# Kernel tuning notes

Measured on AMD Instinct MI355X. Metric: run time of the kernel, lower is better.

Reference implementation:

```python
import jax, jax.numpy as jnp
import numpy as np

B, D, H = 8192, 256, 1024


def setup_inputs() -> dict:
    key = jax.random.key(0)
    ks = jax.random.split(key, 24)
    glorot = lambda k, o, i: jax.random.uniform(k, (o, i), jnp.float32, -1.0, 1.0) * jnp.sqrt(6.0 / (o + i))
    inp = {
        'x': jax.random.normal(ks[0], (B, D), jnp.float32),
        'm': (jax.random.uniform(ks[1], (B, D)) < 0.8).astype(jnp.float32),  # binary observation mask
        'delta': jax.random.uniform(ks[2], (B, D), jnp.float32),             # nonnegative time gaps
        'h': jax.random.normal(ks[3], (B, H), jnp.float32),
        'x_last_obs': jax.random.normal(ks[4], (B, D), jnp.float32),
        'x_mean': jax.random.normal(ks[5], (D,), jnp.float32),
        'W_gamma_x': jax.random.uniform(ks[6], (D,), jnp.float32, 0.001, 0.01),
        'b_gamma_x': jnp.zeros((D,), jnp.float32),
        'W_gamma_h': glorot(ks[7], H, D), 'b_gamma_h': jnp.zeros((H,), jnp.float32),
        'W_xz': glorot(ks[8], H, D), 'W_hz': glorot(ks[9], H, H),
        'W_mz': glorot(ks[10], H, D), 'b_mz': jnp.zeros((H,), jnp.float32),
        'W_xr': glorot(ks[11], H, D), 'W_hr': glorot(ks[12], H, H),
        'W_mr': glorot(ks[13], H, D), 'b_mr': jnp.zeros((H,), jnp.float32),
        'W_xh': glorot(ks[14], H, D), 'W_hh': glorot(ks[15], H, H),
        'W_mh': glorot(ks[16], H, D), 'b_mh': jnp.zeros((H,), jnp.float32),
    }
    return inp


def reference(x, m, delta, h, x_last_obs, x_mean,
              W_gamma_x, b_gamma_x, W_gamma_h, b_gamma_h,
              W_xz, W_hz, W_mz, b_mz,
              W_xr, W_hr, W_mr, b_mr,
              W_xh, W_hh, W_mh, b_mh):
    # input decay (per-feature) and hidden decay (linear of delta)
    gamma_x = jnp.exp(-jax.nn.relu(delta * W_gamma_x + b_gamma_x))        # [B, D]
    gamma_h = jnp.exp(-jax.nn.relu(delta @ W_gamma_h.T + b_gamma_h))     # [B, H]
    # imputation
    x_last_obs_new = jnp.where(m > 0, x, x_last_obs)
    x_imputed = gamma_x * x_last_obs_new + (1.0 - gamma_x) * x_mean
    x_hat = m * x + (1.0 - m) * x_imputed
    h_decayed = gamma_h * h
    # GRU gates (eval mode: no recurrent dropout)
    z = jax.nn.sigmoid(x_hat @ W_xz.T + h_decayed @ W_hz.T + m @ W_mz.T + b_mz)
    r = jax.nn.sigmoid(x_hat @ W_xr.T + h_decayed @ W_hr.T + m @ W_mr.T + b_mr)
    h_tilde = jnp.tanh(x_hat @ W_xh.T + (r * h_decayed) @ W_hh.T + m @ W_mh.T + b_mh)
    h_new = (1.0 - z) * h_decayed + z * h_tilde
    return h_new, x_last_obs_new
```

## Files before the change

kernel.cpp:

```cpp
#include <hip/hip_runtime.h>
#include <cstdint>
#include <cstddef>

typedef unsigned short u16;
typedef __attribute__((ext_vector_type(8))) short s16x8;
typedef __attribute__((ext_vector_type(8))) u16 u16x8;
typedef __attribute__((ext_vector_type(4))) float f32x4;

#define DEV static __device__ __forceinline__
#define GPTR(p) (const __attribute__((address_space(1))) void*)(p)
#define LPTR(p) (__attribute__((address_space(3))) void*)(p)

DEV float b2f(u16 u) { union { unsigned i; float f; } c; c.i = ((unsigned)u) << 16; return c.f; }
DEV u16 f2b(float f) {
  union { float f; unsigned i; } c; c.f = f;
  unsigned r = (c.i + 0x7fffu + ((c.i >> 16) & 1u)) >> 16;
  return (u16)r;
}
DEV float sigm(float x) { return 1.0f / (1.0f + __expf(-x)); }

__global__ __launch_bounds__(256) void pack_w(
    const float* __restrict__ Wxz, const float* __restrict__ Whz, const float* __restrict__ Wmz,
    const float* __restrict__ Wxr, const float* __restrict__ Whr, const float* __restrict__ Wmr,
    const float* __restrict__ Wxh, const float* __restrict__ Whh, const float* __restrict__ Wmh,
    const float* __restrict__ Wgh,
    u16* __restrict__ WZR, u16* __restrict__ WH, u16* __restrict__ WGH)
{
  int t = blockIdx.x * 256 + threadIdx.x;
  const float* src;
  u16* dst;
  if (t < 589824) {
    int row = t / 192;
    int col = (t % 192) * 8;
    int rr = row & 1023;
    const float *wx, *wh, *wm;
    if (row < 1024)      { wx = Wxz; wh = Whz; wm = Wmz; }
    else if (row < 2048) { wx = Wxr; wh = Whr; wm = Wmr; }
    else                 { wx = Wxh; wh = Whh; wm = Wmh; }
    if (col < 256)       src = wx + rr * 256 + col;
    else if (col < 1280) src = wh + (size_t)rr * 1024 + (col - 256);
    else                 src = wm + rr * 256 + (col - 1280);
    dst = (row < 2048) ? (WZR + (size_t)row * 1536 + col)
                       : (WH + (size_t)(row - 2048) * 1536 + col);
  } else {
    int t2 = t - 589824;
    src = Wgh + t2 * 8;
    dst = WGH + t2 * 8;
  }
  f32x4 a = *(const f32x4*)src;
  f32x4 b = *(const f32x4*)(src + 4);
  u16x8 v;
#pragma unroll
  for (int j = 0; j < 4; ++j) { v[j] = f2b(a[j]); v[j + 4] = f2b(b[j]); }
  *(u16x8*)dst = v;
}

__global__ __launch_bounds__(256) void elem_k(
    const float* __restrict__ x, const float* __restrict__ m, const float* __restrict__ delta,
    const float* __restrict__ xlo, const float* __restrict__ x_mean,
    const float* __restrict__ Wgx, const float* __restrict__ bgx,
    u16* __restrict__ X1, u16* __restrict__ Dbf,
    float* __restrict__ out_xlo)
{
  int t = blockIdx.x * 256 + threadIdx.x;
  int row = t >> 5;
  int col = (t & 31) * 8;
  size_t base = (size_t)row * 256 + col;
  u16x8 vxhat, vm16, vd16;
  f32x4 vlnew[2];
#pragma unroll
  for (int half = 0; half < 2; ++half) {
    f32x4 vx = *(const f32x4*)(x + base + half * 4);
    f32x4 vm = *(const f32x4*)(m + base + half * 4);
    f32x4 vd = *(const f32x4*)(delta + base + half * 4);
    f32x4 vl = *(const f32x4*)(xlo + base + half * 4);
    f32x4 vmean = *(const f32x4*)(x_mean + col + half * 4);
    f32x4 vwg = *(const f32x4*)(Wgx + col + half * 4);
    f32x4 vbg = *(const f32x4*)(bgx + col + half * 4);
#pragma unroll
    for (int j = 0; j < 4; ++j) {
      float mf = vm[j];
      float lnew = (mf > 0.5f) ? vx[j] : vl[j];
      vlnew[half][j] = lnew;
      float gx = __expf(-fmaxf(vd[j] * vwg[j] + vbg[j], 0.0f));
      float ximp = gx * lnew + (1.0f - gx) * vmean[j];
      float xhat = mf * vx[j] + (1.0f - mf) * ximp;
      vxhat[half * 4 + j] = f2b(xhat);
      vm16[half * 4 + j] = f2b(mf);
      vd16[half * 4 + j] = f2b(vd[j]);
    }
  }
  size_t r1536 = (size_t)row * 1536;
  *(u16x8*)(X1 + r1536 + col) = vxhat;
  *(u16x8*)(X1 + r1536 + 1280 + col) = vm16;
  *(u16x8*)(Dbf + base) = vd16;
  *(f32x4*)(out_xlo + base) = vlnew[0];
  *(f32x4*)(out_xlo + base + 4) = vlnew[1];
}

template<int EPI, int MF>
__global__ __launch_bounds__(512, 2) void gemm_bt(
    const u16* __restrict__ A, const u16* __restrict__ A2, int K,
    const u16* __restrict__ W,
    const float* __restrict__ bias0, const float* __restrict__ bias1,
    const float* __restrict__ auxf,
    const u16* __restrict__ auxb,
    const u16* __restrict__ aux2b,
    u16* __restrict__ out0b,
    u16* __restrict__ out1b,
    float* __restrict__ outf)
{
  constexpr int BM = MF * 32;
  constexpr int GX = (MF == 8) ? 8 : 4;
  constexpr int LA = BM / 64;
  __shared__ alignas(16) u16 As[2][BM * 64];
  __shared__ alignas(16) u16 Bs[2][256 * 64];

  const int tid = threadIdx.x;
  const int lane = tid & 63;
  const int wave = tid >> 6;
  const int wr = wave >> 2;
  const int wc = wave & 3;

  const int d = blockIdx.y * GX + blockIdx.x;
  const int L = ((d & 7) << 5) | (d >> 3);
  const int brow = (L >> ((GX == 8) ? 3 : 2)) * BM;
  const int bcol = (L & (GX - 1)) * 256;
  const int NT = K / 64;

  const int slr = lane >> 3;
  const int scol = ((lane & 7) ^ slr) * 8;
  const int lr = lane & 15, g4 = lane >> 4, l8 = lane & 7;

  f32x4 acc[MF][4];
#pragma unroll
  for (int i = 0; i < MF; ++i)
#pragma unroll
    for (int j = 0; j < 4; ++j) { f32x4 z0 = {0.f, 0.f, 0.f, 0.f}; acc[i][j] = z0; }

  auto stageA = [&](int kt, int bu) {
    const int k0 = kt * 64;
    const u16* Ab; size_t Astr; int co = k0;
    if constexpr (EPI == 2) {
      if (kt >= 4 && kt < 20) { Ab = A2; Astr = 1024; co = k0 - 256; }
      else                    { Ab = A;  Astr = 1536; }
    } else { Ab = A; Astr = (size_t)K; }
#pragma unroll
    for (int j = 0; j < LA; ++j) {
      int rh = (j * 4 + wc) * 8;
      int grow = brow + wr * (BM / 2) + rh + slr;
      __builtin_amdgcn_global_load_lds(
          GPTR(Ab + (size_t)grow * Astr + co + scol),
          LPTR(&As[bu][(wr * (BM / 2) + rh) * 64]), 16, 0, 0);
    }
  };
  auto stageB = [&](int kt, int bu) {
    const int k0 = kt * 64;
    const int gw = wr * 2 + (wc & 1), hb = wc >> 1;
#pragma unroll
    for (int j = 0; j < 4; ++j) {
      int rh = (j * 4 + gw) * 8;
      int grow = bcol + hb * 128 + rh + slr;
      __builtin_amdgcn_global_load_lds(
          GPTR(W + (size_t)grow * (size_t)K + k0 + scol),
          LPTR(&Bs[bu][(hb * 128 + rh) * 64]), 16, 0, 0);
    }
  };

  stageA(0, 0); stageB(0, 0);
  asm volatile("s_waitcnt vmcnt(0)" ::: "memory");
  __builtin_amdgcn_s_barrier();

  for (int kt = 0; kt < NT; ++kt) {
    const int bu = kt & 1;
    const u16* as_ = &As[bu][0];
    const u16* bs_ = &Bs[bu][0];
    s16x8 bfr[4];
#pragma unroll
    for (int ks = 0; ks < 2; ++ks) {
#pragma unroll
      for (int ih = 0; ih < MF / 4; ++ih) {
        const int ph = ks * (MF / 4) + ih;
        const int kc = ((ks * 4 + g4) ^ l8) * 8;
        s16x8 af[4];
        if (ih == 0)
#pragma unroll
          for (int j = 0; j < 4; ++j)
            bfr[j] = *(const s16x8*)&bs_[(wc * 64 + j * 16 + lr) * 64 + kc];
#pragma unroll
        for (int ii = 0; ii < 4; ++ii)
          af[ii] = *(const s16x8*)&as_[(wr * (BM / 2) + (ih * 4 + ii) * 16 + lr) * 64 + kc];
        if (kt + 1 < NT) {
          if (ph == 0) { stageA(kt + 1, bu ^ 1); if (MF == 4) stageB(kt + 1, bu ^ 1); }
          else if (ph == 1 && MF == 8) stageB(kt + 1, bu ^ 1);
        }
        __builtin_amdgcn_sched_barrier(0);
        if (ph == 2 * (MF / 4) - 1 && kt + 1 < NT)
          asm volatile("s_waitcnt vmcnt(0)" ::: "memory");
        __builtin_amdgcn_s_barrier();
        asm volatile("s_waitcnt lgkmcnt(0)" ::: "memory");
        __builtin_amdgcn_sched_barrier(0);
        __builtin_amdgcn_s_setprio(1);
#pragma unroll
        for (int ii = 0; ii < 4; ++ii)
#pragma unroll
          for (int j = 0; j < 4; ++j)
            acc[ih * 4 + ii][j] = __builtin_amdgcn_mfma_f32_16x16x32_bf16(
                af[ii], bfr[j], acc[ih * 4 + ii][j], 0, 0, 0);
        __builtin_amdgcn_s_setprio(0);
        __builtin_amdgcn_sched_barrier(0);
        __builtin_amdgcn_s_barrier();
      }
    }
  }

  const int row0 = brow + wr * (MF * 16) + g4 * 4;
  const int col0 = bcol + wc * 64 + lr;
#pragma unroll
  for (int i = 0; i < MF; ++i) {
#pragma unroll
    for (int j = 0; j < 4; ++j) {
      int c_ = col0 + j * 16;
#pragma unroll
      for (int q = 0; q < 4; ++q) {
        int r_ = row0 + i * 16 + q;
        float v = acc[i][j][q];
        if constexpr (EPI == 0) {
          float p = v + bias0[c_];
          float gh = __expf(-fmaxf(p, 0.0f));
          float hd = gh * auxf[(size_t)r_ * 1024 + c_];
          out0b[(size_t)r_ * 1536 + 256 + c_] = f2b(hd);
        } else if constexpr (EPI == 1) {
          if (c_ < 1024) {
            out0b[(size_t)r_ * 1024 + c_] = f2b(sigm(v + bias0[c_]));
          } else {
            int jc = c_ - 1024;
            float rg = sigm(v + bias1[jc]);
            float hd = b2f(auxb[(size_t)r_ * 1536 + 256 + jc]);
            out1b[(size_t)r_ * 1024 + jc] = f2b(rg * hd);
          }
        } else {
          float ht = tanhf(v + bias0[c_]);
          float zz = b2f(aux2b[(size_t)r_ * 1024 + c_]);
          float hd = b2f(auxb[(size_t)r_ * 1536 + 256 + c_]);
          outf[(size_t)r_ * 1024 + c_] = (1.0f - zz) * hd + zz * ht;
        }
      }
    }
  }
}

extern "C" void kernel_launch(void* const* d_in, const int* in_sizes, int n_in,
                              void* d_out, int out_size, void* d_ws, size_t ws_size,
                              hipStream_t stream)
{
  const float* x     = (const float*)d_in[0];
  const float* m     = (const float*)d_in[1];
  const float* delta = (const float*)d_in[2];
  const float* h     = (const float*)d_in[3];
  const float* xlo   = (const float*)d_in[4];
  const float* xmean = (const float*)d_in[5];
  const float* Wgx   = (const float*)d_in[6];
  const float* bgx   = (const float*)d_in[7];
  const float* Wgh   = (const float*)d_in[8];
  const float* bgh   = (const float*)d_in[9];
  const float* Wxz   = (const float*)d_in[10];
  const float* Whz   = (const float*)d_in[11];
  const float* Wmz   = (const float*)d_in[12];
  const float* bmz   = (const float*)d_in[13];
  const float* Wxr   = (const float*)d_in[14];
  const float* Whr   = (const float*)d_in[15];
  const float* Wmr   = (const float*)d_in[16];
  const float* bmr   = (const float*)d_in[17];
  const float* Wxh   = (const float*)d_in[18];
  const float* Whh   = (const float*)d_in[19];
  const float* Wmh   = (const float*)d_in[20];
  const float* bmh   = (const float*)d_in[21];

  u16* X1  = (u16*)d_ws;
  u16* Z   = X1 + (size_t)8192 * 1536;
  u16* RH  = Z  + (size_t)8192 * 1024;
  u16* WZR = RH + (size_t)8192 * 1024;
  u16* WH  = WZR + (size_t)2048 * 1536;
  u16* Dbf = WH + (size_t)1024 * 1536;
  u16* WGH = Dbf + (size_t)8192 * 256;

  float* out_h   = (float*)d_out;
  float* out_xlo = out_h + (size_t)8192 * 1024;

  pack_w<<<2432, 256, 0, stream>>>(Wxz, Whz, Wmz, Wxr, Whr, Wmr, Wxh, Whh, Wmh, Wgh, WZR, WH, WGH);
  elem_k<<<1024, 256, 0, stream>>>(x, m, delta, xlo, xmean, Wgx, bgx, X1, Dbf, out_xlo);
  gemm_bt<0, 4><<<dim3(4, 64), 512, 0, stream>>>(
      Dbf, nullptr, 256, WGH, bgh, nullptr, h, nullptr, nullptr, X1, nullptr, nullptr);
  gemm_bt<1, 8><<<dim3(8, 32), 512, 0, stream>>>(
      X1, nullptr, 1536, WZR, bmz, bmr, nullptr, X1, nullptr, Z, RH, nullptr);
  gemm_bt<2, 4><<<dim3(4, 64), 512, 0, stream>>>(
      X1, RH, 1536, WH, bmh, nullptr, nullptr, X1, Z, nullptr, nullptr, out_h);
}
```

Measured before the change: 168.4 us.

## Split LDS tiles into K-halves and prefetch two stages ahead with partial waits

```diff
diff --git a/kernel.cpp b/kernel.cpp
--- a/kernel.cpp
+++ b/kernel.cpp
@@ -112,9 +112,10 @@
 {
   constexpr int BM = MF * 32;
   constexpr int GX = (MF == 8) ? 8 : 4;
-  constexpr int LA = BM / 64;
-  __shared__ alignas(16) u16 As[2][BM * 64];
-  __shared__ alignas(16) u16 Bs[2][256 * 64];
+  constexpr int AL = MF / 4;
+  constexpr int NPH = MF / 2;
+  __shared__ alignas(16) u16 As[2][2][BM * 32];
+  __shared__ alignas(16) u16 Bs[2][2][256 * 32];
 
   const int tid = threadIdx.x;
   const int lane = tid & 63;
@@ -124,13 +125,14 @@
 
   const int d = blockIdx.y * GX + blockIdx.x;
   const int L = ((d & 7) << 5) | (d >> 3);
-  const int brow = (L >> ((GX == 8) ? 3 : 2)) * BM;
-  const int bcol = (L & (GX - 1)) * 256;
+  const int brow = (L / GX) * BM;
+  const int bcol = (L % GX) * 256;
   const int NT = K / 64;
 
-  const int slr = lane >> 3;
-  const int scol = ((lane & 7) ^ slr) * 8;
-  const int lr = lane & 15, g4 = lane >> 4, l8 = lane & 7;
+  const int lr = lane & 15, g4 = lane >> 4;
+  const int rchunk = ((g4 ^ ((lr >> 1) & 3)) * 8);
+  const int sr16 = lane >> 2;
+  const int scs = (lane & 3) ^ ((sr16 >> 1) & 3);
 
   f32x4 acc[MF][4];
 #pragma unroll
@@ -138,79 +140,81 @@
 #pragma unroll
     for (int j = 0; j < 4; ++j) { f32x4 z0 = {0.f, 0.f, 0.f, 0.f}; acc[i][j] = z0; }
 
-  auto stageA = [&](int kt, int bu) {
-    const int k0 = kt * 64;
-    const u16* Ab; size_t Astr; int co = k0;
+  auto stA = [&](int st, int bu, int kh) {
+    int stc = st < NT ? st : NT - 1;
+    const u16* Ab; size_t Astr; int co;
     if constexpr (EPI == 2) {
-      if (kt >= 4 && kt < 20) { Ab = A2; Astr = 1024; co = k0 - 256; }
-      else                    { Ab = A;  Astr = 1536; }
-    } else { Ab = A; Astr = (size_t)K; }
-#pragma unroll
-    for (int j = 0; j < LA; ++j) {
-      int rh = (j * 4 + wc) * 8;
-      int grow = brow + wr * (BM / 2) + rh + slr;
+      if (stc >= 4 && stc < 20) { Ab = A2; Astr = 1024; co = stc * 64 + kh * 32 - 256; }
+      else                      { Ab = A;  Astr = 1536; co = stc * 64 + kh * 32; }
+    } else { Ab = A; Astr = (size_t)K; co = stc * 64 + kh * 32; }
+#pragma unroll
+    for (int q = 0; q < AL; ++q) {
+      int rb = (q * 8 + wave) * 16;
       __builtin_amdgcn_global_load_lds(
-          GPTR(Ab + (size_t)grow * Astr + co + scol),
-          LPTR(&As[bu][(wr * (BM / 2) + rh) * 64]), 16, 0, 0);
+          GPTR(Ab + (size_t)(brow + rb + sr16) * Astr + co + scs * 8),
+          LPTR(&As[bu][kh][rb * 32]), 16, 0, 0);
     }
   };
-  auto stageB = [&](int kt, int bu) {
-    const int k0 = kt * 64;
-    const int gw = wr * 2 + (wc & 1), hb = wc >> 1;
-#pragma unroll
-    for (int j = 0; j < 4; ++j) {
-      int rh = (j * 4 + gw) * 8;
-      int grow = bcol + hb * 128 + rh + slr;
+  auto stB = [&](int st, int bu, int kh) {
+    int stc = st < NT ? st : NT - 1;
+    int co = stc * 64 + kh * 32;
+#pragma unroll
+    for (int q = 0; q < 2; ++q) {
+      int rb = (q * 8 + wave) * 16;
       __builtin_amdgcn_global_load_lds(
-          GPTR(W + (size_t)grow * (size_t)K + k0 + scol),
-          LPTR(&Bs[bu][(hb * 128 + rh) * 64]), 16, 0, 0);
+          GPTR(W + (size_t)(bcol + rb + sr16) * (size_t)K + co + scs * 8),
+          LPTR(&Bs[bu][kh][rb * 32]), 16, 0, 0);
     }
   };
 
-  stageA(0, 0); stageB(0, 0);
-  asm volatile("s_waitcnt vmcnt(0)" ::: "memory");
+  stA(0, 0, 0); stB(0, 0, 0);
+  stA(0, 0, 1); stB(0, 0, 1);
+  stA(1, 1, 0); stB(1, 1, 0);
+  if constexpr (MF == 8) asm volatile("s_waitcnt vmcnt(8)" ::: "memory");
+  else                   asm volatile("s_waitcnt vmcnt(6)" ::: "memory");
   __builtin_amdgcn_s_barrier();
 
+  s16x8 bfr[4];
   for (int kt = 0; kt < NT; ++kt) {
     const int bu = kt & 1;
-    const u16* as_ = &As[bu][0];
-    const u16* bs_ = &Bs[bu][0];
-    s16x8 bfr[4];
-#pragma unroll
-    for (int ks = 0; ks < 2; ++ks) {
-#pragma unroll
-      for (int ih = 0; ih < MF / 4; ++ih) {
-        const int ph = ks * (MF / 4) + ih;
-        const int kc = ((ks * 4 + g4) ^ l8) * 8;
-        s16x8 af[4];
-        if (ih == 0)
-#pragma unroll
-          for (int j = 0; j < 4; ++j)
-            bfr[j] = *(const s16x8*)&bs_[(wc * 64 + j * 16 + lr) * 64 + kc];
-#pragma unroll
-        for (int ii = 0; ii < 4; ++ii)
-          af[ii] = *(const s16x8*)&as_[(wr * (BM / 2) + (ih * 4 + ii) * 16 + lr) * 64 + kc];
-        if (kt + 1 < NT) {
-          if (ph == 0) { stageA(kt + 1, bu ^ 1); if (MF == 4) stageB(kt + 1, bu ^ 1); }
-          else if (ph == 1 && MF == 8) stageB(kt + 1, bu ^ 1);
-        }
-        __builtin_amdgcn_sched_barrier(0);
-        if (ph == 2 * (MF / 4) - 1 && kt + 1 < NT)
-          asm volatile("s_waitcnt vmcnt(0)" ::: "memory");
-        __builtin_amdgcn_s_barrier();
-        asm volatile("s_waitcnt lgkmcnt(0)" ::: "memory");
-        __builtin_amdgcn_sched_barrier(0);
-        __builtin_amdgcn_s_setprio(1);
-#pragma unroll
-        for (int ii = 0; ii < 4; ++ii)
-#pragma unroll
-          for (int j = 0; j < 4; ++j)
-            acc[ih * 4 + ii][j] = __builtin_amdgcn_mfma_f32_16x16x32_bf16(
-                af[ii], bfr[j], acc[ih * 4 + ii][j], 0, 0, 0);
-        __builtin_amdgcn_s_setprio(0);
-        __builtin_amdgcn_sched_barrier(0);
-        __builtin_amdgcn_s_barrier();
+#pragma unroll
+    for (int ph = 0; ph < NPH; ++ph) {
+      const int ks = (MF == 8) ? (ph >> 1) : ph;
+      const int mq = (MF == 8) ? (ph & 1) : 0;
+      s16x8 af[4];
+      if (mq == 0)
+#pragma unroll
+        for (int j = 0; j < 4; ++j)
+          bfr[j] = *(const s16x8*)&Bs[bu][ks][(wc * 64 + j * 16 + lr) * 32 + rchunk];
+#pragma unroll
+      for (int ii = 0; ii < 4; ++ii)
+        af[ii] = *(const s16x8*)&As[bu][ks][(wr * (BM / 2) + mq * 64 + ii * 16 + lr) * 32 + rchunk];
+      if constexpr (MF == 8) {
+        if (ph == 0)      stA(kt + 1, bu ^ 1, 1);
+        else if (ph == 1) stB(kt + 1, bu ^ 1, 1);
+        else if (ph == 2) stA(kt + 2, bu, 0);
+        else              stB(kt + 2, bu, 0);
+      } else {
+        if (ph == 0) { stA(kt + 1, bu ^ 1, 1); stB(kt + 1, bu ^ 1, 1); }
+        else         { stA(kt + 2, bu, 0);     stB(kt + 2, bu, 0); }
       }
+      if constexpr (MF == 8) {
+        if (ph & 1) asm volatile("s_waitcnt vmcnt(8)" ::: "memory");
+      } else {
+        asm volatile("s_waitcnt vmcnt(6)" ::: "memory");
+      }
+      __builtin_amdgcn_s_barrier();
+      asm volatile("s_waitcnt lgkmcnt(0)" ::: "memory");
+      __builtin_amdgcn_sched_barrier(0);
+      __builtin_amdgcn_s_setprio(1);
+#pragma unroll
+      for (int ii = 0; ii < 4; ++ii)
+#pragma unroll
+        for (int j = 0; j < 4; ++j)
+          acc[mq * 4 + ii][j] = __builtin_amdgcn_mfma_f32_16x16x32_bf16(
+              af[ii], bfr[j], acc[mq * 4 + ii][j], 0, 0, 0);
+      __builtin_amdgcn_s_setprio(0);
+      __builtin_amdgcn_s_barrier();
     }
   }
 
```

Result: slower. 172.4 us (+2.4%).
